# Kernel optimization log

Measured on AMD Instinct MI355X. Metric: run time of the kernel, lower is better.

The kernel has to match this reference:

```python
import jax, jax.numpy as jnp
import numpy as np

N_HEADS = 16
MAX_LEN = 1024


def setup_inputs() -> dict:
    key = jax.random.key(0)
    ks = jax.random.split(key, 6)
    B, T, C = 4, 1024, 1024
    scale = 0.02
    return {
        "x": jax.random.normal(ks[0], (B, T, C), dtype=jnp.float32),
        "qkv_w": jax.random.normal(ks[1], (3 * C, C), dtype=jnp.float32) * scale,
        "qkv_b": jax.random.normal(ks[2], (3 * C,), dtype=jnp.float32) * scale,
        "proj_w": jax.random.normal(ks[3], (C, C), dtype=jnp.float32) * scale,
        "proj_b": jax.random.normal(ks[4], (C,), dtype=jnp.float32) * scale,
        "rel_pos_emb": jax.random.normal(ks[5], (2 * MAX_LEN - 1, C), dtype=jnp.float32) * scale,
    }


def reference(x, qkv_w, qkv_b, proj_w, proj_b, rel_pos_emb):
    B, T, C = x.shape
    H = N_HEADS
    D = C // H
    # QKV projection: (B,T,3C) -> (3,B,H,T,D)
    qkv = (x @ qkv_w.T + qkv_b).reshape(B, T, 3, H, D)
    qkv = jnp.transpose(qkv, (2, 0, 3, 1, 4))
    q, k, v = qkv[0], qkv[1], qkv[2]
    # scores: (B,H,T,T)
    att = jnp.einsum("bhtd,bhsd->bhts", q, k) / np.sqrt(D).astype(np.float32)
    # Relative position bias: gather-then-sum == sum-then-gather over head_dim.
    # Pre-reduce table to (2*max_len-1, H) to avoid materializing (T,T,C).
    table = rel_pos_emb.reshape(2 * MAX_LEN - 1, H, D).sum(axis=-1)  # (2L-1, H)
    pos = jnp.arange(T)
    rel_idx = pos[:, None] - pos[None, :] + (MAX_LEN - 1)  # (T,T)
    bias = jnp.transpose(table[rel_idx], (2, 0, 1))  # (H,T,T)
    att = att + bias[None]
    # causal mask: positions j > i masked to -inf
    causal = pos[None, :] > pos[:, None]  # (T,T) True above diagonal
    att = jnp.where(causal[None, None], -jnp.inf, att)
    att = jax.nn.softmax(att, axis=-1)
    out = jnp.einsum("bhts,bhsd->bhtd", att, v)  # (B,H,T,D)
    out = jnp.transpose(out, (0, 2, 1, 3)).reshape(B, T, C)
    return out @ proj_w.T + proj_b
```

## Files before the change

kernel.cpp:

```cpp
#include <hip/hip_runtime.h>
#include <hip/hip_bf16.h>
#include <cstdint>


typedef __bf16 bf16x8 __attribute__((ext_vector_type(8)));
typedef float f32x4 __attribute__((ext_vector_type(4)));
typedef float f32x16 __attribute__((ext_vector_type(16)));

__device__ __forceinline__ float bf2f(unsigned short u) {
    return __uint_as_float(((unsigned)u) << 16);
}
__device__ __forceinline__ unsigned short f2bf(float f) {
    __hip_bfloat16 h = __float2bfloat16(f);
    return *reinterpret_cast<unsigned short*>(&h);
}
__device__ __forceinline__ unsigned pk2(float a, float b) {
    return (unsigned)f2bf(a) | ((unsigned)f2bf(b) << 16);
}
__device__ __forceinline__ int4 cvt8(float4 a, float4 b) {
    union { unsigned short s[8]; int4 v; } u;
    u.s[0] = f2bf(a.x); u.s[1] = f2bf(a.y); u.s[2] = f2bf(a.z); u.s[3] = f2bf(a.w);
    u.s[4] = f2bf(b.x); u.s[5] = f2bf(b.y); u.s[6] = f2bf(b.z); u.s[7] = f2bf(b.w);
    return u.v;
}

__device__ __forceinline__ void gload16(const void* g, void* l) {
    __builtin_amdgcn_global_load_lds(
        reinterpret_cast<const __attribute__((address_space(1))) unsigned int*>(
            reinterpret_cast<uintptr_t>(g)),
        reinterpret_cast<__attribute__((address_space(3))) unsigned int*>(
            reinterpret_cast<uintptr_t>(l)),
        16, 0, 0);
}

__global__ __launch_bounds__(256) void cvt3(const float* __restrict__ x,
                                            const float* __restrict__ w1,
                                            const float* __restrict__ w2,
                                            unsigned short* __restrict__ ox,
                                            unsigned short* __restrict__ ow1,
                                            unsigned short* __restrict__ ow2) {
    const int i = blockIdx.x * 256 + threadIdx.x;
    const float* s; unsigned short* d; int li;
    if (i < 524288)      { s = x;  d = ox;  li = i; }
    else if (i < 917504) { s = w1; d = ow1; li = i - 524288; }
    else                 { s = w2; d = ow2; li = i - 917504; }
    const float4 a = *(const float4*)(s + (size_t)li * 8);
    const float4 b = *(const float4*)(s + (size_t)li * 8 + 4);
    *(int4*)(d + (size_t)li * 8) = cvt8(a, b);
}

__global__ __launch_bounds__(256) void table_reduce(const float* __restrict__ rel,
                                                    float* __restrict__ table) {
    const int p = blockIdx.x;
    const int tid = threadIdx.x, lane = tid & 63, wave = tid >> 6;
    const float* r = rel + (size_t)p * 1024;
    float s[4];
#pragma unroll
    for (int k = 0; k < 4; ++k) s[k] = r[tid + 256 * k];
#pragma unroll
    for (int k = 0; k < 4; ++k) {
        float v = s[k];
        for (int o = 32; o; o >>= 1) v += __shfl_xor(v, o, 64);
        if (lane == 0) table[p * 16 + wave + 4 * k] = v;
    }
}

template <int EPI>
__global__ __launch_bounds__(512) void gemm_bt(const unsigned short* __restrict__ A,
                                               const unsigned short* __restrict__ B,
                                               const float* __restrict__ bias,
                                               unsigned short* __restrict__ outb,
                                               float* __restrict__ outf,
                                               int M, int N, int K) {
    __shared__ __attribute__((aligned(16))) unsigned short As[128 * 32];
    __shared__ __attribute__((aligned(16))) unsigned short Bs[128 * 32];
    const int bm = blockIdx.x * 128, bn = blockIdx.y * 128;
    const int tid = threadIdx.x, lane = tid & 63, wave = tid >> 6;
    const int wr = wave & 1, wc = wave >> 1;
    const int quad = lane >> 4, lm = lane & 15;

    const int srow = tid >> 2;
    const int scol = (tid & 3) * 8;
    const unsigned short* Ap = A + (size_t)(bm + srow) * K + scol;
    const unsigned short* Bp = B + (size_t)(bn + srow) * K + scol;
    unsigned short* AsW = &As[tid * 8];
    unsigned short* BsW = &Bs[tid * 8];

    f32x4 acc[4][2];
#pragma unroll
    for (int r = 0; r < 4; ++r)
#pragma unroll
        for (int c = 0; c < 2; ++c) acc[r][c] = (f32x4){0.f, 0.f, 0.f, 0.f};

    for (int kk = 0; kk < K; kk += 32) {
        gload16(Ap + kk, AsW);
        gload16(Bp + kk, BsW);
        __syncthreads();

        bf16x8 af[4], bfr[2];
#pragma unroll
        for (int r = 0; r < 4; ++r)
            af[r] = *(const bf16x8*)(&As[(64 * wr + 16 * r + lm) * 32 + quad * 8]);
#pragma unroll
        for (int c = 0; c < 2; ++c)
            bfr[c] = *(const bf16x8*)(&Bs[(32 * wc + 16 * c + lm) * 32 + quad * 8]);
#pragma unroll
        for (int r = 0; r < 4; ++r)
#pragma unroll
            for (int c = 0; c < 2; ++c)
                acc[r][c] = __builtin_amdgcn_mfma_f32_16x16x32_bf16(af[r], bfr[c], acc[r][c], 0, 0, 0);
        __syncthreads();
    }

#pragma unroll
    for (int r = 0; r < 4; ++r)
#pragma unroll
        for (int c = 0; c < 2; ++c)
#pragma unroll
            for (int i = 0; i < 4; ++i) {
                const int row = bm + 64 * wr + 16 * r + quad * 4 + i;
                const int col = bn + 32 * wc + 16 * c + lm;
                const float v = acc[r][c][i] + bias[col];
                if (EPI == 0) {
                    const int b = row >> 10, t = row & 1023;
                    const int s3 = col >> 10, rem = col & 1023;
                    const int h = rem >> 6, d = rem & 63;
                    const size_t base = (((size_t)s3 * 4 + b) * 16 + h) * 65536;
                    const size_t off = base + (s3 == 2 ? (size_t)d * 1024 + t
                                                       : (size_t)t * 64 + d);
                    outb[off] = f2bf(v);
                } else {
                    outf[(size_t)row * N + col] = v;
                }
            }
}

#define LOADK(DST, KT)                                                        \
    do {                                                                      \
        const unsigned short* kr_ = Kg + (size_t)((KT) * 32 + l5) * 64 + hi8; \
        DST[0] = *(const bf16x8*)(kr_);                                       \
        DST[1] = *(const bf16x8*)(kr_ + 16);                                  \
        DST[2] = *(const bf16x8*)(kr_ + 32);                                  \
        DST[3] = *(const bf16x8*)(kr_ + 48);                                  \
    } while (0)

#define ATTN_TILE(KF, KT)                                                     \
    do {                                                                      \
        const int kt_ = (KT);                                                 \
        const int jb = kt_ * 32;                                              \
         \
        const unsigned short* vb_ = Vtg + (size_t)l5 * 1024 + jb + hi8;       \
        const bf16x8 vf00 = *(const bf16x8*)(vb_);                            \
        const bf16x8 vf01 = *(const bf16x8*)(vb_ + 16);                       \
        const bf16x8 vf10 = *(const bf16x8*)(vb_ + 32768);                    \
        const bf16x8 vf11 = *(const bf16x8*)(vb_ + 32768 + 16);               \
                                    \
        f32x16 s = {0.f};                                                     \
        _Pragma("unroll")                                                     \
        for (int t = 0; t < 4; ++t)                                           \
            s = __builtin_amdgcn_mfma_f32_32x32x16_bf16(KF[t], qf[t], s, 0, 0, 0); \
         \
        float p[16];                                                          \
        _Pragma("unroll")                                                     \
        for (int reg = 0; reg < 16; ++reg) {                                  \
            const int j = jb + (reg & 3) + 8 * (reg >> 2) + 4 * hi;           \
            p[reg] = fmaf(s[reg], 0.125f, tb[q - j + 127]);                   \
        }                                                                     \
        if (jb + 31 > qbase) {         \
            _Pragma("unroll")                                                 \
            for (int reg = 0; reg < 16; ++reg) {                              \
                const int j = jb + (reg & 3) + 8 * (reg >> 2) + 4 * hi;       \
                p[reg] = (j <= q) ? p[reg] : -1e30f;                          \
            }                                                                 \
        }                                                                     \
                                  \
        float mx = p[0];                                                      \
        _Pragma("unroll")                                                     \
        for (int reg = 1; reg < 16; ++reg) mx = fmaxf(mx, p[reg]);            \
        mx = fmaxf(mx, __shfl_xor(mx, 32, 64));                               \
        const float mnew = fmaxf(mi, mx);                                     \
        const float alpha = __expf(mi - mnew);                                \
        mi = mnew;                                                            \
        float lsum = 0.f;                                                     \
        _Pragma("unroll")                                                     \
        for (int reg = 0; reg < 16; ++reg) {                                  \
            p[reg] = __expf(p[reg] - mnew);                                   \
            lsum += p[reg];                                                   \
        }                                                                     \
        li = li * alpha + lsum;     \
                \
        const unsigned P0 = pk2(p[0], p[1]),   P1 = pk2(p[2], p[3]);          \
        const unsigned P2 = pk2(p[4], p[5]),   P3 = pk2(p[6], p[7]);          \
        const unsigned P4 = pk2(p[8], p[9]),   P5 = pk2(p[10], p[11]);        \
        const unsigned P6 = pk2(p[12], p[13]), P7 = pk2(p[14], p[15]);        \
        const unsigned R0 = __shfl_xor(hi ? P0 : P2, 32, 64);                 \
        const unsigned R1 = __shfl_xor(hi ? P1 : P3, 32, 64);                 \
        const unsigned R2 = __shfl_xor(hi ? P4 : P6, 32, 64);                 \
        const unsigned R3 = __shfl_xor(hi ? P5 : P7, 32, 64);                 \
        union { unsigned w[4]; bf16x8 v; } bq0, bq1;                          \
        bq0.w[0] = hi ? R0 : P0;  bq0.w[1] = hi ? R1 : P1;                    \
        bq0.w[2] = hi ? P2 : R0;  bq0.w[3] = hi ? P3 : R1;                    \
        bq1.w[0] = hi ? R2 : P4;  bq1.w[1] = hi ? R3 : P5;                    \
        bq1.w[2] = hi ? P6 : R2;  bq1.w[3] = hi ? P7 : R3;                    \
                                 \
        _Pragma("unroll")                                                     \
        for (int reg = 0; reg < 16; ++reg) {                                  \
            oa0[reg] *= alpha;                                                \
            oa1[reg] *= alpha;                                                \
        }                                                                     \
                        \
        oa0 = __builtin_amdgcn_mfma_f32_32x32x16_bf16(vf00, bq0.v, oa0, 0, 0, 0); \
        oa0 = __builtin_amdgcn_mfma_f32_32x32x16_bf16(vf01, bq1.v, oa0, 0, 0, 0); \
        oa1 = __builtin_amdgcn_mfma_f32_32x32x16_bf16(vf10, bq0.v, oa1, 0, 0, 0); \
        oa1 = __builtin_amdgcn_mfma_f32_32x32x16_bf16(vf11, bq1.v, oa1, 0, 0, 0); \
    } while (0)

__global__ __launch_bounds__(128) void attn_mfma(const unsigned short* __restrict__ qkvb,
                                                 const float* __restrict__ table,
                                                 unsigned short* __restrict__ y) {
    const int bh = blockIdx.x, b = bh >> 4, h = bh & 15;
    const int level = 15 - blockIdx.y;
    const int tid = threadIdx.x, lane = tid & 63, wave = tid >> 6;
    const int l5 = lane & 31, hi = lane >> 5, hi8 = hi * 8;

    __shared__ float tb[1152];

    const unsigned short* Qg  = qkvb + ((size_t)(b)*16 + h) * 65536;
    const unsigned short* Kg  = qkvb + ((size_t)(4 + b)*16 + h) * 65536;
    const unsigned short* Vtg = qkvb + ((size_t)(8 + b)*16 + h) * 65536;

    const int qbase = 64 * level + 32 * wave;
    const int q = qbase + l5;
    const int nt = 2 * level + wave + 1;

    bf16x8 qf[4];
    {
        const unsigned short* qr = Qg + (size_t)q * 64 + hi8;
#pragma unroll
        for (int t = 0; t < 4; ++t) qf[t] = *(const bf16x8*)(qr + t * 16);
    }

    const int tbn = 64 * level + 191;
    for (int i = tid; i < tbn; i += 128) tb[i] = table[(896 + i) * 16 + h];
    __syncthreads();

    f32x16 oa0 = {0.f}, oa1 = {0.f};
    float mi = -1e30f, li = 0.f;

    bf16x8 kA[4], kB[4];
    LOADK(kA, 0);
    int kt = 0;
    for (; kt + 2 <= nt; kt += 2) {
        LOADK(kB, kt + 1);
        ATTN_TILE(kA, kt);
        if (kt + 2 < nt) LOADK(kA, kt + 2);
        ATTN_TILE(kB, kt + 1);
    }
    if (kt < nt) ATTN_TILE(kA, kt);

    li += __shfl_xor(li, 32, 64);
    const float linv = 1.0f / li;
    unsigned short* yq = y + ((size_t)(b * 1024 + q)) * 1024 + h * 64;
#pragma unroll
    for (int g = 0; g < 4; ++g) {
        union { unsigned short u[4]; int2 v; } o4a, o4b;
#pragma unroll
        for (int i = 0; i < 4; ++i) {
            o4a.u[i] = f2bf(oa0[4 * g + i] * linv);
            o4b.u[i] = f2bf(oa1[4 * g + i] * linv);
        }
        *(int2*)(yq + 8 * g + 4 * hi) = o4a.v;
        *(int2*)(yq + 32 + 8 * g + 4 * hi) = o4b.v;
    }
}

extern "C" void kernel_launch(void* const* d_in, const int* in_sizes, int n_in,
                              void* d_out, int out_size, void* d_ws, size_t ws_size,
                              hipStream_t stream) {
    const float* x      = (const float*)d_in[0];
    const float* qkv_w  = (const float*)d_in[1];
    const float* qkv_b  = (const float*)d_in[2];
    const float* proj_w = (const float*)d_in[3];
    const float* proj_b = (const float*)d_in[4];
    const float* rel    = (const float*)d_in[5];
    float* out = (float*)d_out;

    char* ws = (char*)d_ws;
    unsigned short* xb   = (unsigned short*)(ws + 0);
    unsigned short* qwb  = (unsigned short*)(ws + 8388608);
    unsigned short* pwb  = (unsigned short*)(ws + 14680064);
    float* table         = (float*)(ws + 16777216);
    unsigned short* qkvb = (unsigned short*)(ws + 16908288);
    unsigned short* yb   = (unsigned short*)(ws + 42074112);

    cvt3<<<4096, 256, 0, stream>>>(x, qkv_w, proj_w, xb, qwb, pwb);
    table_reduce<<<2047, 256, 0, stream>>>(rel, table);
    gemm_bt<0><<<dim3(32, 24), 512, 0, stream>>>(xb, qwb, qkv_b, qkvb, nullptr,
                                                 4096, 3072, 1024);
    attn_mfma<<<dim3(64, 16), 128, 0, stream>>>(qkvb, table, yb);
    gemm_bt<1><<<dim3(32, 8), 512, 0, stream>>>(yb, pwb, proj_b, nullptr, out,
                                                4096, 1024, 1024);
}
```

Before: 197.7 us.

## Process two key tiles per softmax step and skip rescaling when max barely changes

The attention inner loop now handles two 32-key tiles at once. Both QK MFMAs are issued together, the next K tiles are prefetched after them, and one combined row max and softmax update covers both tiles, halving the per-tile reduction and rescale overhead. It also adds lazy rescaling: the running max and the output accumulators are only updated when some lane's new max exceeds the old one by more than 8. This removes most of the alpha multiplies but lets exponentials reach up to e^8 before a rescale, which relies on float range and accepts extra register pressure from the larger unroll.

```diff
diff --git a/kernel.cpp b/kernel.cpp
--- a/kernel.cpp
+++ b/kernel.cpp
@@ -146,49 +146,51 @@
 
 #define ATTN_TILE(KF, KT)                                                     \
     do {                                                                      \
-        const int kt_ = (KT);                                                 \
-        const int jb = kt_ * 32;                                              \
-         \
+        const int jb = (KT) * 32;                                             \
         const unsigned short* vb_ = Vtg + (size_t)l5 * 1024 + jb + hi8;       \
         const bf16x8 vf00 = *(const bf16x8*)(vb_);                            \
         const bf16x8 vf01 = *(const bf16x8*)(vb_ + 16);                       \
         const bf16x8 vf10 = *(const bf16x8*)(vb_ + 32768);                    \
         const bf16x8 vf11 = *(const bf16x8*)(vb_ + 32768 + 16);               \
-                                    \
         f32x16 s = {0.f};                                                     \
         _Pragma("unroll")                                                     \
         for (int t = 0; t < 4; ++t)                                           \
             s = __builtin_amdgcn_mfma_f32_32x32x16_bf16(KF[t], qf[t], s, 0, 0, 0); \
-         \
         float p[16];                                                          \
         _Pragma("unroll")                                                     \
         for (int reg = 0; reg < 16; ++reg) {                                  \
             const int j = jb + (reg & 3) + 8 * (reg >> 2) + 4 * hi;           \
             p[reg] = fmaf(s[reg], 0.125f, tb[q - j + 127]);                   \
         }                                                                     \
-        if (jb + 31 > qbase) {         \
+        if (jb + 31 > qbase) {                                                \
             _Pragma("unroll")                                                 \
             for (int reg = 0; reg < 16; ++reg) {                              \
                 const int j = jb + (reg & 3) + 8 * (reg >> 2) + 4 * hi;       \
                 p[reg] = (j <= q) ? p[reg] : -1e30f;                          \
             }                                                                 \
         }                                                                     \
-                                  \
         float mx = p[0];                                                      \
         _Pragma("unroll")                                                     \
         for (int reg = 1; reg < 16; ++reg) mx = fmaxf(mx, p[reg]);            \
         mx = fmaxf(mx, __shfl_xor(mx, 32, 64));                               \
-        const float mnew = fmaxf(mi, mx);                                     \
-        const float alpha = __expf(mi - mnew);                                \
-        mi = mnew;                                                            \
+        if (!__all(mx <= mi + 8.f)) {                                         \
+            const float mnew = fmaxf(mi, mx);                                 \
+            const float alpha = __expf(mi - mnew);                            \
+            mi = mnew;                                                        \
+            li *= alpha;                                                      \
+            _Pragma("unroll")                                                 \
+            for (int reg = 0; reg < 16; ++reg) {                              \
+                oa0[reg] *= alpha;                                            \
+                oa1[reg] *= alpha;                                            \
+            }                                                                 \
+        }                                                                     \
         float lsum = 0.f;                                                     \
         _Pragma("unroll")                                                     \
         for (int reg = 0; reg < 16; ++reg) {                                  \
-            p[reg] = __expf(p[reg] - mnew);                                   \
+            p[reg] = __expf(p[reg] - mi);                                     \
             lsum += p[reg];                                                   \
         }                                                                     \
-        li = li * alpha + lsum;     \
-                \
+        li += lsum;                                                           \
         const unsigned P0 = pk2(p[0], p[1]),   P1 = pk2(p[2], p[3]);          \
         const unsigned P2 = pk2(p[4], p[5]),   P3 = pk2(p[6], p[7]);          \
         const unsigned P4 = pk2(p[8], p[9]),   P5 = pk2(p[10], p[11]);        \
@@ -202,17 +204,107 @@
         bq0.w[2] = hi ? P2 : R0;  bq0.w[3] = hi ? P3 : R1;                    \
         bq1.w[0] = hi ? R2 : P4;  bq1.w[1] = hi ? R3 : P5;                    \
         bq1.w[2] = hi ? P6 : R2;  bq1.w[3] = hi ? P7 : R3;                    \
-                                 \
-        _Pragma("unroll")                                                     \
-        for (int reg = 0; reg < 16; ++reg) {                                  \
-            oa0[reg] *= alpha;                                                \
-            oa1[reg] *= alpha;                                                \
-        }                                                                     \
-                        \
         oa0 = __builtin_amdgcn_mfma_f32_32x32x16_bf16(vf00, bq0.v, oa0, 0, 0, 0); \
         oa0 = __builtin_amdgcn_mfma_f32_32x32x16_bf16(vf01, bq1.v, oa0, 0, 0, 0); \
         oa1 = __builtin_amdgcn_mfma_f32_32x32x16_bf16(vf10, bq0.v, oa1, 0, 0, 0); \
         oa1 = __builtin_amdgcn_mfma_f32_32x32x16_bf16(vf11, bq1.v, oa1, 0, 0, 0); \
+    } while (0)
+
+#define PACKP(p, BQA, BQB)                                                    \
+    do {                                                                      \
+        const unsigned P0 = pk2(p[0], p[1]),   P1 = pk2(p[2], p[3]);          \
+        const unsigned P2 = pk2(p[4], p[5]),   P3 = pk2(p[6], p[7]);          \
+        const unsigned P4 = pk2(p[8], p[9]),   P5 = pk2(p[10], p[11]);        \
+        const unsigned P6 = pk2(p[12], p[13]), P7 = pk2(p[14], p[15]);        \
+        const unsigned R0 = __shfl_xor(hi ? P0 : P2, 32, 64);                 \
+        const unsigned R1 = __shfl_xor(hi ? P1 : P3, 32, 64);                 \
+        const unsigned R2 = __shfl_xor(hi ? P4 : P6, 32, 64);                 \
+        const unsigned R3 = __shfl_xor(hi ? P5 : P7, 32, 64);                 \
+        BQA.w[0] = hi ? R0 : P0;  BQA.w[1] = hi ? R1 : P1;                    \
+        BQA.w[2] = hi ? P2 : R0;  BQA.w[3] = hi ? P3 : R1;                    \
+        BQB.w[0] = hi ? R2 : P4;  BQB.w[1] = hi ? R3 : P5;                    \
+        BQB.w[2] = hi ? P6 : R2;  BQB.w[3] = hi ? P7 : R3;                    \
+    } while (0)
+
+#define ATTN_TILE2(KT)                                                        \
+    do {                                                                      \
+        const int jb = (KT) * 32;                                             \
+                \
+        const unsigned short* vb_ = Vtg + (size_t)l5 * 1024 + jb + hi8;       \
+        const bf16x8 vf00 = *(const bf16x8*)(vb_);                            \
+        const bf16x8 vf01 = *(const bf16x8*)(vb_ + 16);                       \
+        const bf16x8 vf02 = *(const bf16x8*)(vb_ + 32);                       \
+        const bf16x8 vf03 = *(const bf16x8*)(vb_ + 48);                       \
+        const bf16x8 vf10 = *(const bf16x8*)(vb_ + 32768);                    \
+        const bf16x8 vf11 = *(const bf16x8*)(vb_ + 32768 + 16);               \
+        const bf16x8 vf12 = *(const bf16x8*)(vb_ + 32768 + 32);               \
+        const bf16x8 vf13 = *(const bf16x8*)(vb_ + 32768 + 48);               \
+                        \
+        f32x16 s0v = {0.f}, s1v = {0.f};                                      \
+        _Pragma("unroll")                                                     \
+        for (int t = 0; t < 4; ++t) {                                         \
+            s0v = __builtin_amdgcn_mfma_f32_32x32x16_bf16(kA[t], qf[t], s0v, 0, 0, 0); \
+            s1v = __builtin_amdgcn_mfma_f32_32x32x16_bf16(kB[t], qf[t], s1v, 0, 0, 0); \
+        }                                                                     \
+                  \
+        if ((KT) + 2 < nt) LOADK(kA, (KT) + 2);                               \
+        if ((KT) + 3 < nt) LOADK(kB, (KT) + 3);                               \
+                                                 \
+        float p0[16], p1[16];                                                 \
+        _Pragma("unroll")                                                     \
+        for (int reg = 0; reg < 16; ++reg) {                                  \
+            const int jo = (reg & 3) + 8 * (reg >> 2) + 4 * hi;               \
+            p0[reg] = fmaf(s0v[reg], 0.125f, tb[q - jb - jo + 127]);          \
+            p1[reg] = fmaf(s1v[reg], 0.125f, tb[q - jb - 32 - jo + 127]);     \
+        }                                                                     \
+        if (jb + 63 > qbase) {                                                \
+            _Pragma("unroll")                                                 \
+            for (int reg = 0; reg < 16; ++reg) {                              \
+                const int jo = (reg & 3) + 8 * (reg >> 2) + 4 * hi;           \
+                p0[reg] = (jb + jo <= q) ? p0[reg] : -1e30f;                  \
+                p1[reg] = (jb + 32 + jo <= q) ? p1[reg] : -1e30f;             \
+            }                                                                 \
+        }                                                                     \
+                               \
+        float mx = p0[0];                                                     \
+        _Pragma("unroll")                                                     \
+        for (int reg = 1; reg < 16; ++reg) mx = fmaxf(mx, p0[reg]);           \
+        _Pragma("unroll")                                                     \
+        for (int reg = 0; reg < 16; ++reg) mx = fmaxf(mx, p1[reg]);           \
+        mx = fmaxf(mx, __shfl_xor(mx, 32, 64));                               \
+                  \
+        if (!__all(mx <= mi + 8.f)) {                                         \
+            const float mnew = fmaxf(mi, mx);                                 \
+            const float alpha = __expf(mi - mnew);                            \
+            mi = mnew;                                                        \
+            li *= alpha;                                                      \
+            _Pragma("unroll")                                                 \
+            for (int reg = 0; reg < 16; ++reg) {                              \
+                oa0[reg] *= alpha;                                            \
+                oa1[reg] *= alpha;                                            \
+            }                                                                 \
+        }                                                                     \
+        float lsum = 0.f;                                                     \
+        _Pragma("unroll")                                                     \
+        for (int reg = 0; reg < 16; ++reg) {                                  \
+            p0[reg] = __expf(p0[reg] - mi);                                   \
+            p1[reg] = __expf(p1[reg] - mi);                                   \
+            lsum += p0[reg] + p1[reg];                                        \
+        }                                                                     \
+        li += lsum;                                                           \
+                                  \
+        union { unsigned w[4]; bf16x8 v; } bq00, bq01, bq10, bq11;            \
+        PACKP(p0, bq00, bq01);                                                \
+        PACKP(p1, bq10, bq11);                                                \
+                                \
+        oa0 = __builtin_amdgcn_mfma_f32_32x32x16_bf16(vf00, bq00.v, oa0, 0, 0, 0); \
+        oa1 = __builtin_amdgcn_mfma_f32_32x32x16_bf16(vf10, bq00.v, oa1, 0, 0, 0); \
+        oa0 = __builtin_amdgcn_mfma_f32_32x32x16_bf16(vf01, bq01.v, oa0, 0, 0, 0); \
+        oa1 = __builtin_amdgcn_mfma_f32_32x32x16_bf16(vf11, bq01.v, oa1, 0, 0, 0); \
+        oa0 = __builtin_amdgcn_mfma_f32_32x32x16_bf16(vf02, bq10.v, oa0, 0, 0, 0); \
+        oa1 = __builtin_amdgcn_mfma_f32_32x32x16_bf16(vf12, bq10.v, oa1, 0, 0, 0); \
+        oa0 = __builtin_amdgcn_mfma_f32_32x32x16_bf16(vf03, bq11.v, oa0, 0, 0, 0); \
+        oa1 = __builtin_amdgcn_mfma_f32_32x32x16_bf16(vf13, bq11.v, oa1, 0, 0, 0); \
     } while (0)
 
 __global__ __launch_bounds__(128) void attn_mfma(const unsigned short* __restrict__ qkvb,
@@ -249,13 +341,9 @@
 
     bf16x8 kA[4], kB[4];
     LOADK(kA, 0);
+    LOADK(kB, nt > 1 ? 1 : 0);
     int kt = 0;
-    for (; kt + 2 <= nt; kt += 2) {
-        LOADK(kB, kt + 1);
-        ATTN_TILE(kA, kt);
-        if (kt + 2 < nt) LOADK(kA, kt + 2);
-        ATTN_TILE(kB, kt + 1);
-    }
+    for (; kt + 1 < nt; kt += 2) ATTN_TILE2(kt);
     if (kt < nt) ATTN_TILE(kA, kt);
 
     li += __shfl_xor(li, 32, 64);
```

After: 193.4 us. 2.2% less time.
